# Optimization experiments

Hardware: AMD Instinct MI355X
Metric: run time of the kernel (lower is better)

The kernel has to match this reference:

```python
import jax, jax.numpy as jnp
import numpy as np

NUM_EXPERTS = 4  # matches init_kwargs

def setup_inputs() -> dict:
    key = jax.random.key(0)
    ks = jax.random.split(key, 6)
    B, T, D = 4, 4096, 1024
    H = 4 * D
    x = jax.random.normal(ks[0], (B, T, D), dtype=jnp.float32)
    token_mask = jax.random.randint(ks[1], (B, T), 0, NUM_EXPERTS, dtype=jnp.int32)
    s1 = 1.0 / np.sqrt(D)
    s2 = 1.0 / np.sqrt(H)
    W1 = jax.random.normal(ks[2], (H, D), dtype=jnp.float32) * s1
    b1 = jax.random.normal(ks[3], (H,), dtype=jnp.float32) * s1
    W2 = jax.random.normal(ks[4], (D, H), dtype=jnp.float32) * s2
    b2 = jax.random.normal(ks[5], (D,), dtype=jnp.float32) * s2
    return {"x": x, "token_mask": token_mask, "W1": W1, "b1": b1, "W2": W2, "b2": b2}

def reference(x, token_mask, W1, b1, W2, b2):
    # Nested MoE FFN: expert m uses leading D//2^(E-1-m) input dims and
    # leading H//2^(E-1-m) hidden dims; top expert (m=E-1) is the full MLP.
    D = x.shape[-1]
    H = W1.shape[0]
    factor = 2 ** (NUM_EXPERTS - 1 - token_mask)          # [B,T] int
    d_in = D // factor                                     # [B,T]
    d_hid = H // factor                                    # [B,T]
    mask_in = (jnp.arange(D) < d_in[..., None]).astype(x.dtype)    # [B,T,D]
    mask_hid = (jnp.arange(H) < d_hid[..., None]).astype(x.dtype)  # [B,T,H]
    # Expand: slice input dims, project, keep only nested hidden slice (bias included only there)
    h = (jnp.einsum('btd,hd->bth', x * mask_in, W1) + b1) * mask_hid
    h = jax.nn.gelu(h, approximate=False)  # gelu(0)=0 preserves nested zeros
    # Contract: zeros outside the nested hidden slice contribute nothing; full output + bias
    out = jnp.einsum('bth,dh->btd', h, W2) + b2
    return out
```

## Files before the change

### kernel.cpp

```cpp
#include <hip/hip_runtime.h>
#include <cstdint>
#include <math.h>

typedef __attribute__((ext_vector_type(8))) __bf16 bf16x8;
typedef __attribute__((ext_vector_type(4))) float f32x4;
typedef unsigned short ushort_t;

__device__ __forceinline__ ushort_t f2bf(float f) {
    uint32_t u = __float_as_uint(f);
    u += 0x7fff + ((u >> 16) & 1);
    return (ushort_t)(u >> 16);
}

__device__ __forceinline__ float gelu_fast(float x) {
    float u = x * (0.7978845608f + 0.0356774081f * x * x);
    float e = __expf(2.0f * u);
    float th = 1.0f - 2.0f / (e + 1.0f);
    return 0.5f * x * (1.0f + th);
}

__device__ __forceinline__ float gelu_exact(float v) {
    return 0.5f * v * (1.0f + erff(v * 0.70710678118654752440f));
}

__global__ void histo_convw_kernel(const int* __restrict__ tm, int* __restrict__ cnt,
                                   int nchunks,
                                   const float* __restrict__ s1, const float* __restrict__ s2,
                                   ushort_t* __restrict__ d1, ushort_t* __restrict__ d2,
                                   int n4) {
    if (blockIdx.x < (unsigned)nchunks) {
        __shared__ int h[4];
        if (threadIdx.x < 4) h[threadIdx.x] = 0;
        __syncthreads();
        int e = tm[blockIdx.x * 256 + threadIdx.x];
        atomicAdd(&h[e], 1);
        __syncthreads();
        if (threadIdx.x < 4) cnt[blockIdx.x * 4 + threadIdx.x] = h[threadIdx.x];
    } else {
        const int stride = (gridDim.x - nchunks) * 256;
        for (int i = (blockIdx.x - nchunks) * 256 + threadIdx.x; i < 2 * n4; i += stride) {
            const float* src; ushort_t* dst; int k;
            if (i < n4) { src = s1; dst = d1; k = i; }
            else        { src = s2; dst = d2; k = i - n4; }
            const float4 v = ((const float4*)src)[k];
            ushort4 o;
            o.x = f2bf(v.x); o.y = f2bf(v.y); o.z = f2bf(v.z); o.w = f2bf(v.w);
            ((ushort4*)dst)[k] = o;
        }
    }
}

__global__ void meta_kernel(int* __restrict__ meta, int* __restrict__ cnt,
                            int* __restrict__ sidx, int nchunks, int D, int H) {
    __shared__ int tot[4];
    __shared__ int soff_s[4];
    const int t = threadIdx.x;
    const int e = t >> 6;
    const int c0 = t & 63;
    int carry = 0;
    for (int base = 0; base < nchunks; base += 64) {
        int c = base + c0;
        int v = (c < nchunks) ? cnt[c * 4 + e] : 0;
        int s = v;
#pragma unroll
        for (int d = 1; d < 64; d <<= 1) {
            int y = __shfl_up(s, d);
            if (c0 >= d) s += y;
        }
        if (c < nchunks) cnt[c * 4 + e] = s - v + carry;
        carry += __shfl(s, 63);
    }
    if (c0 == 0) tot[e] = carry;
    __syncthreads();
    if (t == 0) {
        int off = 0, xoff = 0, hoff = 0;
        for (int ee = 0; ee < 4; ee++) {
            int c = tot[ee];
            int ac = (c + 127) & ~127;
            meta[ee] = c; meta[4 + ee] = off; meta[8 + ee] = ac; meta[12 + ee] = ac >> 7;
            meta[16 + ee] = xoff; meta[20 + ee] = hoff;
            soff_s[ee] = off;
            off += ac; xoff += ac * (D >> (3 - ee)); hoff += ac * (H >> (3 - ee));
        }
        meta[28] = off;
        int a = 0, b = 0;
        for (int k = 0; k < 4; k++) {
            int ee = 3 - k;
            meta[24 + k] = a; a += meta[12 + ee] * ((H >> (3 - ee)) >> 7);
            meta[32 + k] = b; b += meta[12 + ee] * (D >> 7);
        }
        meta[29] = a; meta[36] = b;
        meta[48] = 0;
        meta[49] = 0;
    }
    __syncthreads();
    for (int base = 0; base < 64 * ((nchunks + 63) / 64); base += 64) {
        int c = base + c0;
        if (c < nchunks) cnt[c * 4 + e] += soff_s[e];
    }
    for (int ee = 0; ee < 4; ee++) {
        int s0 = soff_s[ee] + tot[ee];
        int n = meta[8 + ee] - tot[ee];
        for (int i = t; i < n; i += 256) sidx[s0 + i] = -1;
    }
}

__global__ void place_kernel(const int* __restrict__ tm, const int* __restrict__ cofs,
                             int* __restrict__ sidx) {
    __shared__ unsigned char se[256];
    const int c = blockIdx.x;
    const int t = threadIdx.x;
    const int tok = c * 256 + t;
    const int e = tm[tok];
    se[t] = (unsigned char)e;
    __syncthreads();
    int rank = 0;
    for (int i = 0; i < t; i++) rank += (se[i] == (unsigned char)e);
    sidx[cofs[c * 4 + e] + rank] = tok;
}

__global__ void convert_x_sorted(const float* __restrict__ x,
                                 const int* __restrict__ meta,
                                 const int* __restrict__ sidx,
                                 ushort_t* __restrict__ xb, int D) {
    const int rows = meta[28];
    for (int p = blockIdx.x; p < rows; p += gridDim.x) {
        const int e = (p >= meta[5]) + (p >= meta[6]) + (p >= meta[7]);
        const int off = meta[4 + e];
        const int din = D >> (3 - e);
        const int tok = sidx[p];
        ushort_t* dst = xb + (size_t)meta[16 + e] + (size_t)(p - off) * din;
        const int c = threadIdx.x * 4;
        if (c < din) {
            if (tok < 0) {
                *(ushort4*)(dst + c) = ushort4{0, 0, 0, 0};
            } else {
                const float4 v = *(const float4*)(x + (size_t)tok * D + c);
                ushort4 o;
                o.x = f2bf(v.x); o.y = f2bf(v.y); o.z = f2bf(v.z); o.w = f2bf(v.w);
                *(ushort4*)(dst + c) = o;
            }
        }
    }
}

__device__ __forceinline__ void stage4(const ushort_t* Ag, const ushort_t* Bg,
                                       int lda, int ldb,
                                       char* AsB, char* BsB, int ldsoff) {
    __builtin_amdgcn_global_load_lds(
        (__attribute__((address_space(1))) void*)(uintptr_t)Ag,
        (__attribute__((address_space(3))) void*)(AsB + ldsoff), 16, 0, 0);
    __builtin_amdgcn_global_load_lds(
        (__attribute__((address_space(1))) void*)(uintptr_t)(Ag + (size_t)64 * lda),
        (__attribute__((address_space(3))) void*)(AsB + 4096 + ldsoff), 16, 0, 0);
    __builtin_amdgcn_global_load_lds(
        (__attribute__((address_space(1))) void*)(uintptr_t)Bg,
        (__attribute__((address_space(3))) void*)(BsB + ldsoff), 16, 0, 0);
    __builtin_amdgcn_global_load_lds(
        (__attribute__((address_space(1))) void*)(uintptr_t)(Bg + (size_t)64 * ldb),
        (__attribute__((address_space(3))) void*)(BsB + 4096 + ldsoff), 16, 0, 0);
}

template <int EPI>
__global__ void gemm_sorted(const ushort_t* __restrict__ Abuf,
                            const ushort_t* __restrict__ Bw,
                            const float* __restrict__ bias,
                            const int* meta,
                            const int* __restrict__ sidx,
                            ushort_t* __restrict__ hb,
                            float* __restrict__ out,
                            int* tctr,
                            int D, int H) {
    __shared__ ushort_t As[3][128 * 32];
    __shared__ ushort_t Bs[3][128 * 32];
    __shared__ int s_next;

    const int t    = threadIdx.x;
    const int wave = t >> 6;
    const int lane = t & 63;
    const int quad = lane >> 4;
    const int l16  = lane & 15;
    const int wm   = wave & 1;
    const int wn   = wave >> 1;
    const int srow = t >> 2;
    const int scol = (((t & 3) ^ ((t >> 3) & 3)) * 8);
    const int ldsoff = wave * 64 * 16;
    const int qa = (quad ^ ((l16 >> 1) & 3)) * 8;

    const int* st = meta + (EPI == 0 ? 24 : 32);
    const int  T  = meta[EPI == 0 ? 29 : 36];

    while (true) {
        if (t == 0) s_next = atomicAdd(tctr, 1);
        __syncthreads();
        const int idx = s_next;
        if (idx >= T) break;

        const int k3 = (idx >= st[1]) + (idx >= st[2]) + (idx >= st[3]);
        const int e = 3 - k3;
        const int local = idx - st[k3];
        const int mtiles = meta[12 + e];
        const int mt = local % mtiles;
        const int nt = local / mtiles;

        const int K   = (EPI == 0) ? (D >> (3 - e)) : (H >> (3 - e));
        const int Ne  = (EPI == 0) ? (H >> (3 - e)) : D;
        const int lda = K;
        const int ldb = (EPI == 0) ? D : H;
        const int nb  = nt * 128;
        const ushort_t* A = Abuf + (size_t)((EPI == 0) ? meta[16 + e] : meta[20 + e]);

        const ushort_t* Ag = A + (size_t)(mt * 128 + srow) * lda + scol;
        const ushort_t* Bg = Bw + (size_t)(nb + srow) * ldb + scol;

        const int nsteps = K >> 5;

        f32x4 acc[4][4] = {};

        stage4(Ag,      Bg,      lda, ldb, (char*)As[0], (char*)Bs[0], ldsoff);
        stage4(Ag + 32, Bg + 32, lda, ldb, (char*)As[1], (char*)Bs[1], ldsoff);
        stage4(Ag + 64, Bg + 64, lda, ldb, (char*)As[2], (char*)Bs[2], ldsoff);

        int cur = 0;
        for (int s = 0; s < nsteps; ++s) {
            const int rem = nsteps - s;
            if (rem > 2)       { asm volatile("s_waitcnt vmcnt(8)" ::: "memory"); }
            else if (rem == 2) { asm volatile("s_waitcnt vmcnt(4)" ::: "memory"); }
            else               { asm volatile("s_waitcnt vmcnt(0)" ::: "memory"); }
            __builtin_amdgcn_s_barrier();
            asm volatile("" ::: "memory");

            bf16x8 af[4], bfr[4];
#pragma unroll
            for (int i = 0; i < 4; i++) {
                af[i]  = *(const bf16x8*)(As[cur] + (wm * 64 + i * 16 + l16) * 32 + qa);
                bfr[i] = *(const bf16x8*)(Bs[cur] + (wn * 64 + i * 16 + l16) * 32 + qa);
            }
            asm volatile("s_waitcnt lgkmcnt(0)" ::: "memory");
            __builtin_amdgcn_s_barrier();
            asm volatile("" ::: "memory");

            if (s + 3 < nsteps)
                stage4(Ag + (size_t)(s + 3) * 32, Bg + (size_t)(s + 3) * 32,
                       lda, ldb, (char*)As[cur], (char*)Bs[cur], ldsoff);

#pragma unroll
            for (int i = 0; i < 4; i++)
#pragma unroll
                for (int j = 0; j < 4; j++)
                    acc[i][j] = __builtin_amdgcn_mfma_f32_16x16x32_bf16(af[i], bfr[j], acc[i][j], 0, 0, 0);

            cur = (cur == 2) ? 0 : cur + 1;
        }

        const int colbase = nb + wn * 64 + l16;
        float bv[4];
#pragma unroll
        for (int j = 0; j < 4; j++) bv[j] = bias[colbase + j * 16];

#pragma unroll
        for (int i = 0; i < 4; i++) {
#pragma unroll
            for (int r = 0; r < 4; r++) {
                const int lrow = mt * 128 + wm * 64 + i * 16 + quad * 4 + r;
                if (EPI == 0) {
                    ushort_t* dst = hb + (size_t)meta[20 + e] + (size_t)lrow * Ne;
#pragma unroll
                    for (int j = 0; j < 4; j++)
                        dst[colbase + j * 16] = f2bf(gelu_fast(acc[i][j][r] + bv[j]));
                } else {
                    const int tok = sidx[meta[4 + e] + lrow];
                    if (tok >= 0) {
                        float* dst = out + (size_t)tok * D;
#pragma unroll
                        for (int j = 0; j < 4; j++)
                            dst[colbase + j * 16] = acc[i][j][r] + bv[j];
                    }
                }
            }
        }
        __syncthreads();
    }
}

__global__ void naive_kernel(const float* __restrict__ x, const int* __restrict__ tm,
                             const float* __restrict__ W1, const float* __restrict__ b1,
                             const float* __restrict__ W2, const float* __restrict__ b2,
                             float* __restrict__ out, int D, int Hdim) {
    const int t = blockIdx.x;
    const int m = tm[t];
    const int din = D >> (3 - m);
    const int dh = Hdim >> (3 - m);
    extern __shared__ float sm[];
    float* xs = sm;
    float* hs = sm + D;
    for (int i = threadIdx.x; i < din; i += blockDim.x) xs[i] = x[(size_t)t * D + i];
    __syncthreads();
    for (int h = threadIdx.x; h < dh; h += blockDim.x) {
        const float* w = W1 + (size_t)h * D;
        float a = b1[h];
        for (int d = 0; d < din; d++) a += xs[d] * w[d];
        hs[h] = gelu_exact(a);
    }
    __syncthreads();
    for (int d = threadIdx.x; d < D; d += blockDim.x) {
        const float* w = W2 + (size_t)d * Hdim;
        float a = b2[d];
        for (int h = 0; h < dh; h++) a += hs[h] * w[h];
        out[(size_t)t * D + d] = a;
    }
}

extern "C" void kernel_launch(void* const* d_in, const int* in_sizes, int n_in,
                              void* d_out, int out_size, void* d_ws, size_t ws_size,
                              hipStream_t stream) {
    const float* x  = (const float*)d_in[0];
    const int* tm   = (const int*)d_in[1];
    const float* W1 = (const float*)d_in[2];
    const float* b1 = (const float*)d_in[3];
    const float* W2 = (const float*)d_in[4];
    const float* b2 = (const float*)d_in[5];
    float* out = (float*)d_out;

    const int M    = in_sizes[1];
    const int Hdim = in_sizes[3];
    const int D    = in_sizes[0] / M;

    const int Mpad = M + 512;
    const int nchunks = M / 256;
    const size_t meta_sz = 256;
    const size_t cnt_sz  = ((size_t)nchunks * 4 * 4 + 255) & ~(size_t)255;
    const size_t sidx_sz = ((size_t)Mpad * 4 + 255) & ~(size_t)255;
    const size_t xb_sz   = (size_t)Mpad * D * 2;
    const size_t w1_sz   = (size_t)Hdim * D * 2;
    const size_t w2_sz   = (size_t)D * Hdim * 2;
    const size_t hb_sz   = (size_t)Mpad * Hdim * 2;
    const size_t need_sorted = meta_sz + cnt_sz + sidx_sz + xb_sz + w1_sz + w2_sz + hb_sz;

    const bool shape_ok = (M % 256 == 0) && (D % 128 == 0) && (Hdim % 128 == 0) &&
                          (D >= 1024) && (D <= 1024) && (Hdim >= 4096);

    if (shape_ok && ws_size >= need_sorted) {
        char* p = (char*)d_ws;
        int* meta     = (int*)p;        p += meta_sz;
        int* cnt      = (int*)p;        p += cnt_sz;
        int* sidx     = (int*)p;        p += sidx_sz;
        ushort_t* xb  = (ushort_t*)p;   p += xb_sz;
        ushort_t* w1b = (ushort_t*)p;   p += w1_sz;
        ushort_t* w2b = (ushort_t*)p;   p += w2_sz;
        ushort_t* hb  = (ushort_t*)p;

        const int n4w = Hdim * D / 4;
        histo_convw_kernel<<<nchunks + 2048, 256, 0, stream>>>(tm, cnt, nchunks,
                                                               W1, W2, w1b, w2b, n4w);
        meta_kernel<<<1, 256, 0, stream>>>(meta, cnt, sidx, nchunks, D, Hdim);
        place_kernel<<<nchunks, 256, 0, stream>>>(tm, cnt, sidx);
        convert_x_sorted<<<2048, 256, 0, stream>>>(x, meta, sidx, xb, D);

        gemm_sorted<0><<<768, 256, 0, stream>>>(xb, w1b, b1, meta, sidx, hb, nullptr,
                                                meta + 48, D, Hdim);
        gemm_sorted<1><<<768, 256, 0, stream>>>(hb, w2b, b2, meta, sidx, nullptr, out,
                                                meta + 49, D, Hdim);
        return;
    }

    const size_t shmem = (size_t)(D + Hdim) * sizeof(float);
    naive_kernel<<<M, 256, shmem, stream>>>(x, tm, W1, b1, W2, b2, out, D, Hdim);
}
```

Before: 357.1 us.

## Split-K the largest expert's second GEMM with atomics and double-buffer LDS

The second GEMM's work for the top expert (K=4096) is split into two K halves. Each half accumulates into the output with atomicAdd, and the output is pre-filled with b2 inside the x-conversion kernel. This is meant to balance tile lengths across the persistent grid. The LDS pipeline drops from three buffers to two, the XOR swizzle on LDS reads is removed, and the grid grows from 768 to 1024 blocks to raise occupancy. The costs are float atomics, possible LDS bank conflicts without the swizzle, shallower prefetch, and non-deterministic summation order.

Measured after the change: 382.0 us. 7.0% more time.

```diff
diff --git a/kernel.cpp b/kernel.cpp
--- a/kernel.cpp
+++ b/kernel.cpp
@@ -87,7 +87,7 @@
         for (int k = 0; k < 4; k++) {
             int ee = 3 - k;
             meta[24 + k] = a; a += meta[12 + ee] * ((H >> (3 - ee)) >> 7);
-            meta[32 + k] = b; b += meta[12 + ee] * (D >> 7);
+            meta[32 + k] = b; b += meta[12 + ee] * (D >> 7) * (ee == 3 ? 2 : 1);
         }
         meta[29] = a; meta[36] = b;
         meta[48] = 0;
@@ -122,7 +122,10 @@
 __global__ void convert_x_sorted(const float* __restrict__ x,
                                  const int* __restrict__ meta,
                                  const int* __restrict__ sidx,
-                                 ushort_t* __restrict__ xb, int D) {
+                                 ushort_t* __restrict__ xb,
+                                 const float* __restrict__ b2,
+                                 float* __restrict__ out,
+                                 int Mtok, int D) {
     const int rows = meta[28];
     for (int p = blockIdx.x; p < rows; p += gridDim.x) {
         const int e = (p >= meta[5]) + (p >= meta[6]) + (p >= meta[7]);
@@ -142,6 +145,13 @@
             }
         }
     }
+    const int d4 = D >> 2;
+    const int total4 = Mtok * d4;
+    const float4* b24 = (const float4*)b2;
+    float4* out4 = (float4*)out;
+    for (int i = blockIdx.x * blockDim.x + threadIdx.x; i < total4;
+         i += gridDim.x * blockDim.x)
+        out4[i] = b24[i & (d4 - 1)];
 }
 
 __device__ __forceinline__ void stage4(const ushort_t* Ag, const ushort_t* Bg,
@@ -171,8 +181,8 @@
                             float* __restrict__ out,
                             int* tctr,
                             int D, int H) {
-    __shared__ ushort_t As[3][128 * 32];
-    __shared__ ushort_t Bs[3][128 * 32];
+    __shared__ ushort_t As[2][128 * 32];
+    __shared__ ushort_t Bs[2][128 * 32];
     __shared__ int s_next;
 
     const int t    = threadIdx.x;
@@ -183,9 +193,8 @@
     const int wm   = wave & 1;
     const int wn   = wave >> 1;
     const int srow = t >> 2;
-    const int scol = (((t & 3) ^ ((t >> 3) & 3)) * 8);
+    const int scol = (t & 3) * 8;
     const int ldsoff = wave * 64 * 16;
-    const int qa = (quad ^ ((l16 >> 1) & 3)) * 8;
 
     const int* st = meta + (EPI == 0 ? 24 : 32);
     const int  T  = meta[EPI == 0 ? 29 : 36];
@@ -198,50 +207,51 @@
 
         const int k3 = (idx >= st[1]) + (idx >= st[2]) + (idx >= st[3]);
         const int e = 3 - k3;
-        const int local = idx - st[k3];
+        int local = idx - st[k3];
+        int kh = 0;
+        if (EPI == 1 && e == 3) { kh = local & 1; local >>= 1; }
         const int mtiles = meta[12 + e];
         const int mt = local % mtiles;
         const int nt = local / mtiles;
 
-        const int K   = (EPI == 0) ? (D >> (3 - e)) : (H >> (3 - e));
+        const int Kfull = (EPI == 0) ? (D >> (3 - e)) : (H >> (3 - e));
+        const int Ksub  = (EPI == 1 && e == 3) ? (Kfull >> 1) : Kfull;
         const int Ne  = (EPI == 0) ? (H >> (3 - e)) : D;
-        const int lda = K;
+        const int lda = Kfull;
         const int ldb = (EPI == 0) ? D : H;
         const int nb  = nt * 128;
+        const int koff = kh * Ksub;
         const ushort_t* A = Abuf + (size_t)((EPI == 0) ? meta[16 + e] : meta[20 + e]);
 
-        const ushort_t* Ag = A + (size_t)(mt * 128 + srow) * lda + scol;
-        const ushort_t* Bg = Bw + (size_t)(nb + srow) * ldb + scol;
-
-        const int nsteps = K >> 5;
+        const ushort_t* Ag = A + (size_t)(mt * 128 + srow) * lda + scol + koff;
+        const ushort_t* Bg = Bw + (size_t)(nb + srow) * ldb + scol + koff;
+
+        const int nsteps = Ksub >> 5;
 
         f32x4 acc[4][4] = {};
 
         stage4(Ag,      Bg,      lda, ldb, (char*)As[0], (char*)Bs[0], ldsoff);
         stage4(Ag + 32, Bg + 32, lda, ldb, (char*)As[1], (char*)Bs[1], ldsoff);
-        stage4(Ag + 64, Bg + 64, lda, ldb, (char*)As[2], (char*)Bs[2], ldsoff);
 
         int cur = 0;
         for (int s = 0; s < nsteps; ++s) {
-            const int rem = nsteps - s;
-            if (rem > 2)       { asm volatile("s_waitcnt vmcnt(8)" ::: "memory"); }
-            else if (rem == 2) { asm volatile("s_waitcnt vmcnt(4)" ::: "memory"); }
-            else               { asm volatile("s_waitcnt vmcnt(0)" ::: "memory"); }
+            if (nsteps - s > 1) { asm volatile("s_waitcnt vmcnt(4)" ::: "memory"); }
+            else                { asm volatile("s_waitcnt vmcnt(0)" ::: "memory"); }
             __builtin_amdgcn_s_barrier();
             asm volatile("" ::: "memory");
 
             bf16x8 af[4], bfr[4];
 #pragma unroll
             for (int i = 0; i < 4; i++) {
-                af[i]  = *(const bf16x8*)(As[cur] + (wm * 64 + i * 16 + l16) * 32 + qa);
-                bfr[i] = *(const bf16x8*)(Bs[cur] + (wn * 64 + i * 16 + l16) * 32 + qa);
+                af[i]  = *(const bf16x8*)(As[cur] + (wm * 64 + i * 16 + l16) * 32 + quad * 8);
+                bfr[i] = *(const bf16x8*)(Bs[cur] + (wn * 64 + i * 16 + l16) * 32 + quad * 8);
             }
             asm volatile("s_waitcnt lgkmcnt(0)" ::: "memory");
             __builtin_amdgcn_s_barrier();
             asm volatile("" ::: "memory");
 
-            if (s + 3 < nsteps)
-                stage4(Ag + (size_t)(s + 3) * 32, Bg + (size_t)(s + 3) * 32,
+            if (s + 2 < nsteps)
+                stage4(Ag + (size_t)(s + 2) * 32, Bg + (size_t)(s + 2) * 32,
                        lda, ldb, (char*)As[cur], (char*)Bs[cur], ldsoff);
 
 #pragma unroll
@@ -250,7 +260,7 @@
                 for (int j = 0; j < 4; j++)
                     acc[i][j] = __builtin_amdgcn_mfma_f32_16x16x32_bf16(af[i], bfr[j], acc[i][j], 0, 0, 0);
 
-            cur = (cur == 2) ? 0 : cur + 1;
+            cur ^= 1;
         }
 
         const int colbase = nb + wn * 64 + l16;
@@ -272,9 +282,15 @@
                     const int tok = sidx[meta[4 + e] + lrow];
                     if (tok >= 0) {
                         float* dst = out + (size_t)tok * D;
-#pragma unroll
-                        for (int j = 0; j < 4; j++)
-                            dst[colbase + j * 16] = acc[i][j][r] + bv[j];
+                        if (e == 3) {
+#pragma unroll
+                            for (int j = 0; j < 4; j++)
+                                atomicAdd(&dst[colbase + j * 16], acc[i][j][r]);
+                        } else {
+#pragma unroll
+                            for (int j = 0; j < 4; j++)
+                                dst[colbase + j * 16] = acc[i][j][r] + bv[j];
+                        }
                     }
                 }
             }
@@ -355,12 +371,12 @@
                                                                W1, W2, w1b, w2b, n4w);
         meta_kernel<<<1, 256, 0, stream>>>(meta, cnt, sidx, nchunks, D, Hdim);
         place_kernel<<<nchunks, 256, 0, stream>>>(tm, cnt, sidx);
-        convert_x_sorted<<<2048, 256, 0, stream>>>(x, meta, sidx, xb, D);
-
-        gemm_sorted<0><<<768, 256, 0, stream>>>(xb, w1b, b1, meta, sidx, hb, nullptr,
-                                                meta + 48, D, Hdim);
-        gemm_sorted<1><<<768, 256, 0, stream>>>(hb, w2b, b2, meta, sidx, nullptr, out,
-                                                meta + 49, D, Hdim);
+        convert_x_sorted<<<2048, 256, 0, stream>>>(x, meta, sidx, xb, b2, out, M, D);
+
+        gemm_sorted<0><<<1024, 256, 0, stream>>>(xb, w1b, b1, meta, sidx, hb, nullptr,
+                                                 meta + 48, D, Hdim);
+        gemm_sorted<1><<<1024, 256, 0, stream>>>(hb, w2b, b2, meta, sidx, nullptr, out,
+                                                 meta + 49, D, Hdim);
         return;
     }
 
```
